# Kernel tuning notes

Hardware: AMD Instinct MI355X
Metric: run time of the kernel (lower is better)

The kernel has to match this reference:

```python
import jax, jax.numpy as jnp
import numpy as np

B, S, E, H = 2, 2048, 512, 8
MLP = 4 * E


def _ln(x, w, b, eps=1e-5):
    m = jnp.mean(x, -1, keepdims=True)
    v = jnp.var(x, -1, keepdims=True)
    return (x - m) / jnp.sqrt(v + eps) * w + b


def setup_inputs() -> dict:
    key = jax.random.key(0)
    ks = jax.random.split(key, 8)
    s = lambda k, shape: (jax.random.normal(k, shape, jnp.float32) * 0.02)
    return {
        "query": jax.random.normal(ks[0], (B, S, E), jnp.float32),
        "attn_gate": jax.random.uniform(ks[1], (B * H, S, S), jnp.float32),
        "in_proj_w": s(ks[2], (3 * E, E)),
        "in_proj_b": jnp.zeros((3 * E,), jnp.float32),
        "out_w": s(ks[3], (E, E)),
        "out_b": jnp.zeros((E,), jnp.float32),
        "ln1_w": jnp.ones((E,), jnp.float32),
        "ln1_b": jnp.zeros((E,), jnp.float32),
        "ln2_w": jnp.ones((E,), jnp.float32),
        "ln2_b": jnp.zeros((E,), jnp.float32),
        "w1": s(ks[4], (MLP, E)),
        "b1": jnp.zeros((MLP,), jnp.float32),
        "w2": s(ks[5], (E, MLP)),
        "b2": jnp.zeros((E,), jnp.float32),
    }


def reference(query, attn_gate, in_proj_w, in_proj_b, out_w, out_b,
              ln1_w, ln1_b, ln2_w, ln2_b, w1, b1, w2, b2):
    b, s, e = query.shape
    h = H
    dh = e // h
    nq = _ln(query, ln1_w, ln1_b)  # pre-LN; key=value=normed query (self-attn)
    Wq, Wk, Wv = jnp.split(in_proj_w, 3, axis=0)
    bq, bk, bv = jnp.split(in_proj_b, 3, axis=0)
    q = nq @ Wq.T + bq
    k = nq @ Wk.T + bk
    v = nq @ Wv.T + bv
    # faithful raw reshape (B,S,E)->(B*H,S,Dh), as in the torch .view
    q = q.reshape(b * h, s, dh)
    k = k.reshape(b * h, s, dh)
    v = v.reshape(b * h, s, dh)
    w = jnp.einsum("bqd,bkd->bqk", q, k)  # no 1/sqrt(d) scaling in source
    w = w * attn_gate
    w = w / (jnp.sum(w, -1, keepdims=True) + 1e-12)  # sum-renormalization
    w = jax.nn.softmax(w, axis=-1)
    o = jnp.einsum("bqk,bkd->bqd", w, v)  # (B*H, S, Dh)
    o = jnp.swapaxes(o, 0, 1).reshape(s, b, e)  # faithful transpose+view
    o = o @ out_w.T + out_b
    o = jnp.swapaxes(o, 0, 1)  # back to batch_first (B,S,E)
    x = query + o
    hmid = _ln(x, ln2_w, ln2_b)
    x = x + (jax.nn.gelu(hmid @ w1.T + b1, approximate=False) @ w2.T + b2)
    attn_weights = w.reshape(b, h, s, s).mean(axis=1)  # average_attn_weights=True
    return (x, attn_weights)
```

## Files before the change

kernel.cpp:

```cpp
#include <hip/hip_runtime.h>
#include <cstdint>
#include <cstddef>

typedef __bf16 bf16_t;
typedef __bf16 bf16x8 __attribute__((ext_vector_type(8)));
typedef float  f32x4  __attribute__((ext_vector_type(4)));

#define S_LEN   2048
#define E_DIM   512
#define H_NUM   8
#define DH      64
#define MLP_DIM 2048

static __device__ __forceinline__ unsigned short f2bfu(float f){
  bf16_t h = (bf16_t)f;
  return __builtin_bit_cast(unsigned short, h);
}

static __device__ __forceinline__ float gelu_f(float v){
  return 0.5f*v*(1.0f + erff(v*0.70710678118654752f));
}

__global__ __launch_bounds__(256) void cvt_kernel(const float* __restrict__ s,
                                                  bf16_t* __restrict__ d, int n){
  int i = (blockIdx.x*256 + threadIdx.x)*4;
  if (i < n){
    float4 v = *(const float4*)(s + i);
    ushort4 pk;
    pk.x = f2bfu(v.x); pk.y = f2bfu(v.y); pk.z = f2bfu(v.z); pk.w = f2bfu(v.w);
    *(ushort4*)((unsigned short*)d + i) = pk;
  }
}

__global__ __launch_bounds__(256) void cvt_split_kernel(const float* __restrict__ s,
                                                        bf16_t* __restrict__ dh,
                                                        bf16_t* __restrict__ dl, int n){
  int i = (blockIdx.x*256 + threadIdx.x)*4;
  if (i < n){
    float4 v = *(const float4*)(s + i);
    float xs[4] = {v.x, v.y, v.z, v.w};
    ushort4 ph, pl;
    unsigned short* hp = (unsigned short*)&ph;
    unsigned short* lp = (unsigned short*)&pl;
    #pragma unroll
    for (int j=0;j<4;j++){
      bf16_t hi = (bf16_t)xs[j];
      bf16_t lo = (bf16_t)(xs[j] - (float)hi);
      hp[j] = __builtin_bit_cast(unsigned short, hi);
      lp[j] = __builtin_bit_cast(unsigned short, lo);
    }
    *(ushort4*)((unsigned short*)dh + i) = ph;
    *(ushort4*)((unsigned short*)dl + i) = pl;
  }
}

__global__ __launch_bounds__(256) void ln_kernel(const float* __restrict__ x,
                                                 const float* __restrict__ w,
                                                 const float* __restrict__ bb,
                                                 bf16_t* __restrict__ out){
  const int row  = blockIdx.x*4 + (threadIdx.x>>6);
  const int lane = threadIdx.x & 63;
  const float* xr = x + (size_t)row*E_DIM + lane*8;
  float4 v0 = *(const float4*)xr;
  float4 v1 = *(const float4*)(xr + 4);
  float xs[8] = {v0.x, v0.y, v0.z, v0.w, v1.x, v1.y, v1.z, v1.w};
  float s = 0.f, s2 = 0.f;
  #pragma unroll
  for (int j=0;j<8;j++){ s += xs[j]; s2 += xs[j]*xs[j]; }
  #pragma unroll
  for (int off=1; off<64; off<<=1){
    s  += __shfl_xor(s,  off, 64);
    s2 += __shfl_xor(s2, off, 64);
  }
  float mean = s*(1.f/512.f);
  float var  = s2*(1.f/512.f) - mean*mean;
  float rstd = rsqrtf(fmaxf(var, 0.f) + 1e-5f);
  const float* wp = w  + lane*8;
  const float* bp = bb + lane*8;
  bf16x8 ov;
  #pragma unroll
  for (int j=0;j<8;j++)
    ov[j] = (bf16_t)((xs[j]-mean)*rstd*wp[j] + bp[j]);
  *(bf16x8*)(out + (size_t)row*E_DIM + lane*8) = ov;
}

__global__ __launch_bounds__(256) void ln_split_kernel(const float* __restrict__ x,
                                                       const float* __restrict__ w,
                                                       const float* __restrict__ bb,
                                                       bf16_t* __restrict__ oh,
                                                       bf16_t* __restrict__ ol){
  const int row  = blockIdx.x*4 + (threadIdx.x>>6);
  const int lane = threadIdx.x & 63;
  const float* xr = x + (size_t)row*E_DIM + lane*8;
  float4 v0 = *(const float4*)xr;
  float4 v1 = *(const float4*)(xr + 4);
  float xs[8] = {v0.x, v0.y, v0.z, v0.w, v1.x, v1.y, v1.z, v1.w};
  float s = 0.f, s2 = 0.f;
  #pragma unroll
  for (int j=0;j<8;j++){ s += xs[j]; s2 += xs[j]*xs[j]; }
  #pragma unroll
  for (int off=1; off<64; off<<=1){
    s  += __shfl_xor(s,  off, 64);
    s2 += __shfl_xor(s2, off, 64);
  }
  float mean = s*(1.f/512.f);
  float var  = s2*(1.f/512.f) - mean*mean;
  float rstd = rsqrtf(fmaxf(var, 0.f) + 1e-5f);
  const float* wp = w  + lane*8;
  const float* bp = bb + lane*8;
  bf16x8 vh, vl;
  #pragma unroll
  for (int j=0;j<8;j++){
    float v = (xs[j]-mean)*rstd*wp[j] + bp[j];
    bf16_t hi = (bf16_t)v;
    vh[j] = hi;
    vl[j] = (bf16_t)(v - (float)hi);
  }
  size_t o = (size_t)row*E_DIM + lane*8;
  *(bf16x8*)(oh + o) = vh;
  *(bf16x8*)(ol + o) = vl;
}

__global__ __launch_bounds__(256) void gemm_qkv_split(
    const bf16_t* __restrict__ Ah, const bf16_t* __restrict__ Al,
    const bf16_t* __restrict__ Bh, const bf16_t* __restrict__ Bl,
    const float* __restrict__ bias,
    bf16_t* __restrict__ qh, bf16_t* __restrict__ ql,
    bf16_t* __restrict__ kh, bf16_t* __restrict__ kl,
    bf16_t* __restrict__ vtmp)
{
  constexpr int TM = 128, TN = 64, BK = 64, MI = 4, NI = 2;
  const int K = 512;

  __shared__ bf16_t Ahs[TM*BK], Als[TM*BK];
  __shared__ bf16_t Bhs[TN*BK], Bls[TN*BK];

  const int tid  = threadIdx.x;
  const int wave = tid>>6, lane = tid&63, quad = lane>>4, l16 = lane&15;
  const int wm = wave>>1, wn = wave&1;

  const int nblk = 1536/TN;
  const int bm = blockIdx.x / nblk;
  const int bn = blockIdx.x % nblk;
  const int m0 = bm*TM, n0 = bn*TN;

  f32x4 acc[MI][NI];
  #pragma unroll
  for (int i=0;i<MI;i++)
    #pragma unroll
    for (int j=0;j<NI;j++)
      acc[i][j] = (f32x4){0.f,0.f,0.f,0.f};

  for (int k0 = 0; k0 < K; k0 += BK){
    bf16x8 avh[4], avl[4], bvh[2], bvl[2];
    #pragma unroll
    for (int i=0;i<4;i++){
      int ga = tid + i*256;
      int row = ga>>3, c8 = (ga&7) ^ (row&7);
      size_t off = (size_t)(m0+row)*K + k0 + c8*8;
      avh[i] = *(const bf16x8*)(Ah + off);
      avl[i] = *(const bf16x8*)(Al + off);
    }
    #pragma unroll
    for (int i=0;i<2;i++){
      int gb = tid + i*256;
      int row = gb>>3, c8 = (gb&7) ^ (row&7);
      size_t off = (size_t)(n0+row)*K + k0 + c8*8;
      bvh[i] = *(const bf16x8*)(Bh + off);
      bvl[i] = *(const bf16x8*)(Bl + off);
    }
    __syncthreads();
    #pragma unroll
    for (int i=0;i<4;i++){
      *(bf16x8*)(Ahs + (size_t)(tid + i*256)*8) = avh[i];
      *(bf16x8*)(Als + (size_t)(tid + i*256)*8) = avl[i];
    }
    #pragma unroll
    for (int i=0;i<2;i++){
      *(bf16x8*)(Bhs + (size_t)(tid + i*256)*8) = bvh[i];
      *(bf16x8*)(Bls + (size_t)(tid + i*256)*8) = bvl[i];
    }
    __syncthreads();
    #pragma unroll
    for (int ks=0;ks<2;ks++){
      bf16x8 afh[MI], afl[MI], bfh[NI], bfl[NI];
      #pragma unroll
      for (int mi=0;mi<MI;mi++){
        int rm = wm*64 + mi*16 + l16;
        size_t sl = (size_t)(rm*8 + ((ks*4+quad) ^ (rm&7)))*8;
        afh[mi] = *(const bf16x8*)(Ahs + sl);
        afl[mi] = *(const bf16x8*)(Als + sl);
      }
      #pragma unroll
      for (int ni=0;ni<NI;ni++){
        int rn = wn*32 + ni*16 + l16;
        size_t sl = (size_t)(rn*8 + ((ks*4+quad) ^ (rn&7)))*8;
        bfh[ni] = *(const bf16x8*)(Bhs + sl);
        bfl[ni] = *(const bf16x8*)(Bls + sl);
      }
      #pragma unroll
      for (int mi=0;mi<MI;mi++)
        #pragma unroll
        for (int ni=0;ni<NI;ni++){
          acc[mi][ni] = __builtin_amdgcn_mfma_f32_16x16x32_bf16(afh[mi], bfh[ni], acc[mi][ni], 0,0,0);
          acc[mi][ni] = __builtin_amdgcn_mfma_f32_16x16x32_bf16(afl[mi], bfh[ni], acc[mi][ni], 0,0,0);
          acc[mi][ni] = __builtin_amdgcn_mfma_f32_16x16x32_bf16(afh[mi], bfl[ni], acc[mi][ni], 0,0,0);
        }
    }
  }

  #pragma unroll
  for (int mi=0;mi<MI;mi++){
    const int grow0 = m0 + wm*64 + mi*16 + quad*4;
    #pragma unroll
    for (int ni=0;ni<NI;ni++){
      const int gcol = n0 + wn*32 + ni*16 + l16;
      const float bvx = bias[gcol];
      if (gcol < 512){
        #pragma unroll
        for (int r=0;r<4;r++){
          float v = acc[mi][ni][r] + bvx;
          size_t idx = (size_t)(grow0+r)*E_DIM + gcol;
          bf16_t hi = (bf16_t)v;
          qh[idx] = hi;
          ql[idx] = (bf16_t)(v - (float)hi);
        }
      } else if (gcol < 1024){
        const int cc = gcol - 512;
        #pragma unroll
        for (int r=0;r<4;r++){
          float v = acc[mi][ni][r] + bvx;
          size_t idx = (size_t)(grow0+r)*E_DIM + cc;
          bf16_t hi = (bf16_t)v;
          kh[idx] = hi;
          kl[idx] = (bf16_t)(v - (float)hi);
        }
      } else {
        const int cc = gcol - 1024;
        #pragma unroll
        for (int r=0;r<4;r++)
          vtmp[(size_t)(grow0+r)*E_DIM + cc] = (bf16_t)(acc[mi][ni][r] + bvx);
      }
    }
  }
}

__global__ __launch_bounds__(256) void vtrans_kernel(const bf16_t* __restrict__ v,
                                                     bf16_t* __restrict__ vt){
  __shared__ bf16_t tile[32*516];
  const int ic = blockIdx.x >> 3;
  const int rg = blockIdx.x & 7;
  const int tid = threadIdx.x;
  const size_t src = ((size_t)ic*256 + rg*32)*E_DIM;
  #pragma unroll
  for (int j=0;j<8;j++){
    int idx = j*2048 + tid*8;
    int row = idx >> 9, col = idx & 511;
    *(bf16x8*)(tile + row*516 + col) = *(const bf16x8*)(v + src + idx);
  }
  __syncthreads();
  #pragma unroll
  for (int j=0;j<8;j++){
    int idx = j*2048 + tid*8;
    int d = idx >> 8;
    int toff = idx & 255;
    int row = toff >> 3;
    bf16x8 o;
    #pragma unroll
    for (int jj=0;jj<8;jj++)
      o[jj] = tile[row*516 + jj*64 + d];
    *(bf16x8*)(vt + ((size_t)ic*64 + d)*S_LEN + rg*256 + toff) = o;
  }
}

template<int TN, int MODE>
__global__ __launch_bounds__(256) void gemm_kernel(
    const bf16_t* __restrict__ A, const bf16_t* __restrict__ Bw,
    const float* __restrict__ bias, int M, int N, int K,
    void* out0, const float* __restrict__ resid)
{
  constexpr int TM = 128;
  constexpr int BK = 64;
  constexpr int MI = 4;
  constexpr int NI = TN/32;
  constexpr int GB = TN/32;

  __shared__ bf16_t As[TM*BK];
  __shared__ bf16_t Bs[TN*BK];

  const int tid  = threadIdx.x;
  const int wave = tid>>6, lane = tid&63, quad = lane>>4, l16 = lane&15;
  const int wm = wave>>1, wn = wave&1;

  const int nblk = N / TN;
  const int bm = blockIdx.x / nblk;
  const int bn = blockIdx.x % nblk;
  const int m0 = bm*TM, n0 = bn*TN;

  f32x4 acc[MI][NI];
  #pragma unroll
  for (int i=0;i<MI;i++)
    #pragma unroll
    for (int j=0;j<NI;j++)
      acc[i][j] = (f32x4){0.f,0.f,0.f,0.f};

  for (int k0 = 0; k0 < K; k0 += BK){
    bf16x8 av[4];
    #pragma unroll
    for (int i=0;i<4;i++){
      int ga = tid + i*256;
      int row = ga>>3, c8 = (ga&7) ^ (row&7);
      av[i] = *(const bf16x8*)(A + (size_t)(m0+row)*K + k0 + c8*8);
    }
    bf16x8 bv[GB];
    #pragma unroll
    for (int i=0;i<GB;i++){
      int gb = tid + i*256;
      int row = gb>>3, c8 = (gb&7) ^ (row&7);
      bv[i] = *(const bf16x8*)(Bw + (size_t)(n0+row)*K + k0 + c8*8);
    }
    __syncthreads();
    #pragma unroll
    for (int i=0;i<4;i++)  *(bf16x8*)(As + (size_t)(tid + i*256)*8) = av[i];
    #pragma unroll
    for (int i=0;i<GB;i++) *(bf16x8*)(Bs + (size_t)(tid + i*256)*8) = bv[i];
    __syncthreads();
    #pragma unroll
    for (int ks=0;ks<2;ks++){
      bf16x8 af[MI], bfr[NI];
      #pragma unroll
      for (int mi=0;mi<MI;mi++){
        int rm = wm*64 + mi*16 + l16;
        af[mi] = *(const bf16x8*)(As + (size_t)(rm*8 + ((ks*4+quad) ^ (rm&7)))*8);
      }
      #pragma unroll
      for (int ni=0;ni<NI;ni++){
        int rn = wn*(TN/2) + ni*16 + l16;
        bfr[ni] = *(const bf16x8*)(Bs + (size_t)(rn*8 + ((ks*4+quad) ^ (rn&7)))*8);
      }
      #pragma unroll
      for (int mi=0;mi<MI;mi++)
        #pragma unroll
        for (int ni=0;ni<NI;ni++)
          acc[mi][ni] = __builtin_amdgcn_mfma_f32_16x16x32_bf16(af[mi], bfr[ni], acc[mi][ni], 0,0,0);
    }
  }

  #pragma unroll
  for (int mi=0;mi<MI;mi++){
    const int grow0 = m0 + wm*64 + mi*16 + quad*4;
    #pragma unroll
    for (int ni=0;ni<NI;ni++){
      const int gcol = n0 + wn*(TN/2) + ni*16 + l16;
      const float bvx = bias[gcol];
      if constexpr (MODE==1){
        float* xo = (float*)out0;
        #pragma unroll
        for (int r=0;r<4;r++){
          size_t idx = (size_t)(grow0+r)*E_DIM + gcol;
          xo[idx] = resid[idx] + acc[mi][ni][r] + bvx;
        }
      } else if constexpr (MODE==2){
        bf16_t* hp = (bf16_t*)out0;
        #pragma unroll
        for (int r=0;r<4;r++)
          hp[(size_t)(grow0+r)*MLP_DIM + gcol] = (bf16_t)gelu_f(acc[mi][ni][r] + bvx);
      } else {
        float* xo = (float*)out0;
        #pragma unroll
        for (int r=0;r<4;r++){
          size_t idx = (size_t)(grow0+r)*E_DIM + gcol;
          xo[idx] = xo[idx] + acc[mi][ni][r] + bvx;
        }
      }
    }
  }
}

__global__ __launch_bounds__(512) __attribute__((amdgpu_waves_per_eu(2, 2)))
void attn_kernel(
    const bf16_t* __restrict__ qhb, const bf16_t* __restrict__ qlb,
    const bf16_t* __restrict__ khb, const bf16_t* __restrict__ klb,
    const bf16_t* __restrict__ vt,  const float* __restrict__ gate,
    bf16_t* __restrict__ og, float* __restrict__ aw)
{
  __shared__ __align__(16) float u_s[16*2048];
  __shared__ float osh[16*64];
  __shared__ float zsh[16];

  const int b   = blockIdx.x >> 7;
  const int sqt = blockIdx.x & 127;
  const int sq0 = sqt*16;

  const int tid = threadIdx.x;
  const int wave = tid>>6, lane = tid&63, quad = lane>>4, l16 = lane&15;

  float awacc[64];
  #pragma unroll
  for (int j=0;j<64;j++) awacc[j] = 0.f;

  f32x4 gpre[2][8];
  #pragma unroll
  for (int rr=0;rr<2;rr++){
    const float* gp = gate + ((size_t)(b*H_NUM)*S_LEN + sq0 + wave*2 + rr)*S_LEN + (size_t)lane*4;
    #pragma unroll
    for (int it=0; it<8; it++)
      gpre[rr][it] = __builtin_nontemporal_load((const f32x4*)(gp + it*256));
  }

  for (int h = 0; h < H_NUM; h++){
    const int bh = b*H_NUM + h;

    osh[tid] = 0.f; osh[tid + 512] = 0.f;

    bf16x8 qah0, qah1, qal0, qal1;
    {
      const size_t qoff = ((size_t)bh*S_LEN + sq0 + l16)*DH + quad*8;
      qah0 = *(const bf16x8*)(qhb + qoff);
      qah1 = *(const bf16x8*)(qhb + qoff + 32);
      qal0 = *(const bf16x8*)(qlb + qoff);
      qal1 = *(const bf16x8*)(qlb + qoff + 32);
    }

    for (int cb = wave; cb < 32; cb += 8){
      #pragma unroll
      for (int nb=0; nb<4; nb++){
        const int col0 = cb*64 + nb*16;
        const size_t koff = ((size_t)bh*S_LEN + col0 + l16)*DH + quad*8;
        bf16x8 khf0 = *(const bf16x8*)(khb + koff);
        bf16x8 khf1 = *(const bf16x8*)(khb + koff + 32);
        bf16x8 klf0 = *(const bf16x8*)(klb + koff);
        bf16x8 klf1 = *(const bf16x8*)(klb + koff + 32);
        f32x4 acc = (f32x4){0.f,0.f,0.f,0.f};
        acc = __builtin_amdgcn_mfma_f32_16x16x32_bf16(qah0, khf0, acc, 0,0,0);
        acc = __builtin_amdgcn_mfma_f32_16x16x32_bf16(qah1, khf1, acc, 0,0,0);
        acc = __builtin_amdgcn_mfma_f32_16x16x32_bf16(qal0, khf0, acc, 0,0,0);
        acc = __builtin_amdgcn_mfma_f32_16x16x32_bf16(qal1, khf1, acc, 0,0,0);
        acc = __builtin_amdgcn_mfma_f32_16x16x32_bf16(qah0, klf0, acc, 0,0,0);
        acc = __builtin_amdgcn_mfma_f32_16x16x32_bf16(qah1, klf1, acc, 0,0,0);
        const int c = col0 + l16;
        #pragma unroll
        for (int r=0;r<4;r++){
          const int row = quad*4 + r;
          u_s[row*2048 + (c ^ ((row&7)<<2))] = acc[r];
        }
      }
    }
    __syncthreads();

    #pragma unroll
    for (int rr=0; rr<2; rr++){
      const int row = wave*2 + rr;
      f32x4* ub = (f32x4*)u_s + (size_t)row*512;
      const int sw = row & 7;
      f32x4 uv[8];
      double s = 0.0;
      float mx = -__builtin_inff(), mn = __builtin_inff();
      #pragma unroll
      for (int it=0; it<8; it++){
        uv[it] = ub[(it*64 + lane) ^ sw] * gpre[rr][it];
        s += ((double)uv[it][0] + (double)uv[it][1]) + ((double)uv[it][2] + (double)uv[it][3]);
        mx = fmaxf(mx, fmaxf(fmaxf(uv[it][0],uv[it][1]), fmaxf(uv[it][2],uv[it][3])));
        mn = fminf(mn, fminf(fminf(uv[it][0],uv[it][1]), fminf(uv[it][2],uv[it][3])));
      }
      #pragma unroll
      for (int off=1; off<64; off<<=1){
        s  += __shfl_xor(s, off, 64);
        mx = fmaxf(mx, __shfl_xor(mx, off, 64));
        mn = fminf(mn, __shfl_xor(mn, off, 64));
      }
      const double rsum = s + 1e-12;
      const float inv = (float)(1.0/rsum);
      const float m = (rsum > 0.0 ? mx : mn) * inv;
      float z = 0.f;
      #pragma unroll
      for (int it=0; it<8; it++){
        f32x4 e;
        e[0] = __expf(uv[it][0]*inv - m);
        e[1] = __expf(uv[it][1]*inv - m);
        e[2] = __expf(uv[it][2]*inv - m);
        e[3] = __expf(uv[it][3]*inv - m);
        ub[(it*64 + lane) ^ sw] = e;
        z += (e[0]+e[1]) + (e[2]+e[3]);
      }
      #pragma unroll
      for (int off=1; off<64; off<<=1) z += __shfl_xor(z, off, 64);
      if (lane == 0) zsh[row] = z;
    }
    __syncthreads();

    {
      const int nb2 = wave & 3, khh = wave >> 2;
      f32x4 oacc = (f32x4){0.f,0.f,0.f,0.f};
      const bf16_t* vbase = vt + ((size_t)bh*DH + nb2*16 + l16)*S_LEN;
      const f32x4* ur4 = (const f32x4*)u_s + (size_t)l16*512;
      const int swr = l16 & 7;
      #pragma unroll 4
      for (int kc = khh*32; kc < khh*32 + 32; kc++){
        const int c4a = kc*8 + quad*2;
        f32x4 e0 = ur4[c4a ^ swr];
        f32x4 e1 = ur4[(c4a+1) ^ swr];
        bf16x8 pa;
        pa[0]=(bf16_t)e0[0]; pa[1]=(bf16_t)e0[1]; pa[2]=(bf16_t)e0[2]; pa[3]=(bf16_t)e0[3];
        pa[4]=(bf16_t)e1[0]; pa[5]=(bf16_t)e1[1]; pa[6]=(bf16_t)e1[2]; pa[7]=(bf16_t)e1[3];
        bf16x8 vf = *(const bf16x8*)(vbase + kc*32 + quad*8);
        oacc = __builtin_amdgcn_mfma_f32_16x16x32_bf16(pa, vf, oacc, 0,0,0);
      }
      #pragma unroll
      for (int r=0;r<4;r++)
        atomicAdd(&osh[(quad*4+r)*64 + nb2*16 + l16], oacc[r]);
    }
    __syncthreads();

    #pragma unroll
    for (int t = tid; t < 1024; t += 512){
      int r = t >> 6, d = t & 63;
      float val = osh[t] / zsh[r];
      og[((size_t)(b*S_LEN + sq0 + r))*E_DIM + h*DH + d] = (bf16_t)val;
    }

    if (h + 1 < H_NUM){
      #pragma unroll
      for (int rr=0;rr<2;rr++){
        const float* gp = gate + ((size_t)(b*H_NUM + h + 1)*S_LEN + sq0 + wave*2 + rr)*S_LEN + (size_t)lane*4;
        #pragma unroll
        for (int it=0; it<8; it++)
          gpre[rr][it] = __builtin_nontemporal_load((const f32x4*)(gp + it*256));
      }
    }

    #pragma unroll
    for (int rr=0; rr<2; rr++){
      const int row = wave*2 + rr;
      const float sc = 0.125f / zsh[row];
      const f32x4* ur3 = (const f32x4*)u_s + (size_t)row*512;
      const int sw3 = row & 7;
      #pragma unroll
      for (int g=0; g<8; g++){
        f32x4 e = ur3[(g*64 + lane) ^ sw3];
        awacc[rr*32+g*4+0] = fmaf(e[0], sc, awacc[rr*32+g*4+0]);
        awacc[rr*32+g*4+1] = fmaf(e[1], sc, awacc[rr*32+g*4+1]);
        awacc[rr*32+g*4+2] = fmaf(e[2], sc, awacc[rr*32+g*4+2]);
        awacc[rr*32+g*4+3] = fmaf(e[3], sc, awacc[rr*32+g*4+3]);
      }
    }
    __syncthreads();
  }

  #pragma unroll
  for (int rr=0; rr<2; rr++){
    float* awrow = aw + ((size_t)(b*S_LEN) + sq0 + wave*2 + rr)*S_LEN + (size_t)lane*4;
    #pragma unroll
    for (int g=0; g<8; g++){
      f32x4 v = (f32x4){ awacc[rr*32+g*4+0], awacc[rr*32+g*4+1],
                         awacc[rr*32+g*4+2], awacc[rr*32+g*4+3] };
      __builtin_nontemporal_store(v, (f32x4*)(awrow + g*256));
    }
  }
}

extern "C" void kernel_launch(void* const* d_in, const int* in_sizes, int n_in,
                              void* d_out, int out_size, void* d_ws, size_t ws_size,
                              hipStream_t stream)
{
  const float* query     = (const float*)d_in[0];
  const float* gate      = (const float*)d_in[1];
  const float* in_proj_w = (const float*)d_in[2];
  const float* in_proj_b = (const float*)d_in[3];
  const float* out_w     = (const float*)d_in[4];
  const float* out_b     = (const float*)d_in[5];
  const float* ln1_w     = (const float*)d_in[6];
  const float* ln1_b     = (const float*)d_in[7];
  const float* ln2_w     = (const float*)d_in[8];
  const float* ln2_b     = (const float*)d_in[9];
  const float* w1        = (const float*)d_in[10];
  const float* b1        = (const float*)d_in[11];
  const float* w2        = (const float*)d_in[12];
  const float* b2        = (const float*)d_in[13];

  char* ws = (char*)d_ws;
  bf16_t* nqh   = (bf16_t*)(ws);
  bf16_t* nql   = (bf16_t*)(ws + ((size_t)4<<20));
  bf16_t* qh    = (bf16_t*)(ws + ((size_t)8<<20));
  bf16_t* ql    = (bf16_t*)(ws + ((size_t)12<<20));
  bf16_t* kh    = (bf16_t*)(ws + ((size_t)16<<20));
  bf16_t* kl    = (bf16_t*)(ws + ((size_t)20<<20));
  bf16_t* vtmp  = (bf16_t*)(ws + ((size_t)24<<20));
  bf16_t* vt    = (bf16_t*)(ws + ((size_t)28<<20));
  bf16_t* og    = (bf16_t*)(ws + ((size_t)32<<20));
  bf16_t* hmid  = (bf16_t*)(ws + ((size_t)36<<20));
  bf16_t* h1    = (bf16_t*)(ws + ((size_t)40<<20));
  bf16_t* wqh   = (bf16_t*)(ws + ((size_t)56<<20));
  bf16_t* wql   = (bf16_t*)(ws + ((size_t)58<<20));
  bf16_t* woutb = (bf16_t*)(ws + ((size_t)60<<20));
  bf16_t* w1b   = (bf16_t*)(ws + ((size_t)61<<20));
  bf16_t* w2b   = (bf16_t*)(ws + ((size_t)63<<20));

  float* xout = (float*)d_out;
  float* aw   = xout + (size_t)2*S_LEN*E_DIM;

  cvt_split_kernel<<<768, 256, 0, stream>>>(in_proj_w, wqh, wql, 786432);
  cvt_kernel<<<256, 256, 0, stream>>>(out_w, woutb, 262144);
  cvt_kernel<<<1024,256, 0, stream>>>(w1,    w1b,   1048576);
  cvt_kernel<<<1024,256, 0, stream>>>(w2,    w2b,   1048576);

  ln_split_kernel<<<1024, 256, 0, stream>>>(query, ln1_w, ln1_b, nqh, nql);

  gemm_qkv_split<<<768, 256, 0, stream>>>(nqh, nql, wqh, wql, in_proj_b,
                                          qh, ql, kh, kl, vtmp);

  vtrans_kernel<<<128, 256, 0, stream>>>(vtmp, vt);

  attn_kernel<<<256, 512, 0, stream>>>(qh, ql, kh, kl, vt, gate, og, aw);

  gemm_kernel<64,1><<<256, 256, 0, stream>>>(og, woutb, out_b,
      4096, 512, 512, (void*)xout, query);

  ln_kernel<<<1024, 256, 0, stream>>>(xout, ln2_w, ln2_b, hmid);

  gemm_kernel<128,2><<<512, 256, 0, stream>>>(hmid, w1b, b1,
      4096, 2048, 512, (void*)h1, nullptr);

  gemm_kernel<64,3><<<256, 256, 0, stream>>>(h1, w2b, b2,
      4096, 512, 2048, (void*)xout, nullptr);
}
```

Baseline: 705.8 us.

## Halve attention query tile to 8 rows to double blocks and occupancy

The attention kernel now handles 8 query rows per block instead of 16 and launches 512 blocks. That halves LDS use (64KB instead of 128KB), the awacc registers and the gate prefetch registers, and the waves-per-EU hint goes from 2 to 4. The MFMA tiles stay 16 wide, so half of each QK and PV tile is wasted work on duplicated rows. The next head's gate prefetch moves earlier into the softmax pass, and the gated scores are written back to LDS instead of being held in registers.

```diff
diff --git a/kernel.cpp b/kernel.cpp
--- a/kernel.cpp
+++ b/kernel.cpp
@@ -377,45 +377,44 @@
   }
 }
 
-__global__ __launch_bounds__(512) __attribute__((amdgpu_waves_per_eu(2, 2)))
+__global__ __launch_bounds__(512) __attribute__((amdgpu_waves_per_eu(4, 4)))
 void attn_kernel(
     const bf16_t* __restrict__ qhb, const bf16_t* __restrict__ qlb,
     const bf16_t* __restrict__ khb, const bf16_t* __restrict__ klb,
     const bf16_t* __restrict__ vt,  const float* __restrict__ gate,
     bf16_t* __restrict__ og, float* __restrict__ aw)
 {
-  __shared__ __align__(16) float u_s[16*2048];
-  __shared__ float osh[16*64];
-  __shared__ float zsh[16];
-
-  const int b   = blockIdx.x >> 7;
-  const int sqt = blockIdx.x & 127;
-  const int sq0 = sqt*16;
+  __shared__ __align__(16) float u_s[8*2048];
+  __shared__ float osh[8*64];
+  __shared__ float zsh[8];
+
+  const int b   = blockIdx.x >> 8;
+  const int sqt = blockIdx.x & 255;
+  const int sq0 = sqt*8;
 
   const int tid = threadIdx.x;
   const int wave = tid>>6, lane = tid&63, quad = lane>>4, l16 = lane&15;
 
-  float awacc[64];
-  #pragma unroll
-  for (int j=0;j<64;j++) awacc[j] = 0.f;
-
-  f32x4 gpre[2][8];
-  #pragma unroll
-  for (int rr=0;rr<2;rr++){
-    const float* gp = gate + ((size_t)(b*H_NUM)*S_LEN + sq0 + wave*2 + rr)*S_LEN + (size_t)lane*4;
+  float awacc[32];
+  #pragma unroll
+  for (int j=0;j<32;j++) awacc[j] = 0.f;
+
+  f32x4 gpre[8];
+  {
+    const float* gp = gate + ((size_t)(b*H_NUM)*S_LEN + sq0 + wave)*S_LEN + (size_t)lane*4;
     #pragma unroll
     for (int it=0; it<8; it++)
-      gpre[rr][it] = __builtin_nontemporal_load((const f32x4*)(gp + it*256));
+      gpre[it] = *(const f32x4*)(gp + it*256);
   }
 
   for (int h = 0; h < H_NUM; h++){
     const int bh = b*H_NUM + h;
 
-    osh[tid] = 0.f; osh[tid + 512] = 0.f;
+    osh[tid] = 0.f;
 
     bf16x8 qah0, qah1, qal0, qal1;
     {
-      const size_t qoff = ((size_t)bh*S_LEN + sq0 + l16)*DH + quad*8;
+      const size_t qoff = ((size_t)bh*S_LEN + sq0 + (l16&7))*DH + quad*8;
       qah0 = *(const bf16x8*)(qhb + qoff);
       qah1 = *(const bf16x8*)(qhb + qoff + 32);
       qal0 = *(const bf16x8*)(qlb + qoff);
@@ -439,29 +438,37 @@
         acc = __builtin_amdgcn_mfma_f32_16x16x32_bf16(qah0, klf0, acc, 0,0,0);
         acc = __builtin_amdgcn_mfma_f32_16x16x32_bf16(qah1, klf1, acc, 0,0,0);
         const int c = col0 + l16;
-        #pragma unroll
-        for (int r=0;r<4;r++){
-          const int row = quad*4 + r;
-          u_s[row*2048 + (c ^ ((row&7)<<2))] = acc[r];
+        if (quad < 2){
+          #pragma unroll
+          for (int r=0;r<4;r++){
+            const int row = quad*4 + r;
+            u_s[row*2048 + (c ^ (row<<2))] = acc[r];
+          }
         }
       }
     }
     __syncthreads();
 
-    #pragma unroll
-    for (int rr=0; rr<2; rr++){
-      const int row = wave*2 + rr;
+    {
+      const int row = wave;
       f32x4* ub = (f32x4*)u_s + (size_t)row*512;
-      const int sw = row & 7;
-      f32x4 uv[8];
+      const int sw = row;
       double s = 0.0;
       float mx = -__builtin_inff(), mn = __builtin_inff();
       #pragma unroll
       for (int it=0; it<8; it++){
-        uv[it] = ub[(it*64 + lane) ^ sw] * gpre[rr][it];
-        s += ((double)uv[it][0] + (double)uv[it][1]) + ((double)uv[it][2] + (double)uv[it][3]);
-        mx = fmaxf(mx, fmaxf(fmaxf(uv[it][0],uv[it][1]), fmaxf(uv[it][2],uv[it][3])));
-        mn = fminf(mn, fminf(fminf(uv[it][0],uv[it][1]), fminf(uv[it][2],uv[it][3])));
+        const int c4 = (it*64 + lane) ^ sw;
+        f32x4 u = ub[c4] * gpre[it];
+        ub[c4] = u;
+        s += ((double)u[0] + (double)u[1]) + ((double)u[2] + (double)u[3]);
+        mx = fmaxf(mx, fmaxf(fmaxf(u[0],u[1]), fmaxf(u[2],u[3])));
+        mn = fminf(mn, fminf(fminf(u[0],u[1]), fminf(u[2],u[3])));
+      }
+      if (h + 1 < H_NUM){
+        const float* gp = gate + ((size_t)(b*H_NUM + h + 1)*S_LEN + sq0 + wave)*S_LEN + (size_t)lane*4;
+        #pragma unroll
+        for (int it=0; it<8; it++)
+          gpre[it] = *(const f32x4*)(gp + it*256);
       }
       #pragma unroll
       for (int off=1; off<64; off<<=1){
@@ -475,12 +482,14 @@
       float z = 0.f;
       #pragma unroll
       for (int it=0; it<8; it++){
+        const int c4 = (it*64 + lane) ^ sw;
+        f32x4 u = ub[c4];
         f32x4 e;
-        e[0] = __expf(uv[it][0]*inv - m);
-        e[1] = __expf(uv[it][1]*inv - m);
-        e[2] = __expf(uv[it][2]*inv - m);
-        e[3] = __expf(uv[it][3]*inv - m);
-        ub[(it*64 + lane) ^ sw] = e;
+        e[0] = __expf(u[0]*inv - m);
+        e[1] = __expf(u[1]*inv - m);
+        e[2] = __expf(u[2]*inv - m);
+        e[3] = __expf(u[3]*inv - m);
+        ub[c4] = e;
         z += (e[0]+e[1]) + (e[2]+e[3]);
       }
       #pragma unroll
@@ -493,7 +502,7 @@
       const int nb2 = wave & 3, khh = wave >> 2;
       f32x4 oacc = (f32x4){0.f,0.f,0.f,0.f};
       const bf16_t* vbase = vt + ((size_t)bh*DH + nb2*16 + l16)*S_LEN;
-      const f32x4* ur4 = (const f32x4*)u_s + (size_t)l16*512;
+      const f32x4* ur4 = (const f32x4*)u_s + (size_t)(l16&7)*512;
       const int swr = l16 & 7;
       #pragma unroll 4
       for (int kc = khh*32; kc < khh*32 + 32; kc++){
@@ -506,54 +515,42 @@
         bf16x8 vf = *(const bf16x8*)(vbase + kc*32 + quad*8);
         oacc = __builtin_amdgcn_mfma_f32_16x16x32_bf16(pa, vf, oacc, 0,0,0);
       }
-      #pragma unroll
-      for (int r=0;r<4;r++)
-        atomicAdd(&osh[(quad*4+r)*64 + nb2*16 + l16], oacc[r]);
-    }
-    __syncthreads();
-
-    #pragma unroll
-    for (int t = tid; t < 1024; t += 512){
-      int r = t >> 6, d = t & 63;
-      float val = osh[t] / zsh[r];
+      if (quad < 2){
+        #pragma unroll
+        for (int r=0;r<4;r++)
+          atomicAdd(&osh[(quad*4+r)*64 + nb2*16 + l16], oacc[r]);
+      }
+    }
+    __syncthreads();
+
+    {
+      int r = tid >> 6, d = tid & 63;
+      float val = osh[tid] / zsh[r];
       og[((size_t)(b*S_LEN + sq0 + r))*E_DIM + h*DH + d] = (bf16_t)val;
     }
 
-    if (h + 1 < H_NUM){
-      #pragma unroll
-      for (int rr=0;rr<2;rr++){
-        const float* gp = gate + ((size_t)(b*H_NUM + h + 1)*S_LEN + sq0 + wave*2 + rr)*S_LEN + (size_t)lane*4;
-        #pragma unroll
-        for (int it=0; it<8; it++)
-          gpre[rr][it] = __builtin_nontemporal_load((const f32x4*)(gp + it*256));
-      }
-    }
-
-    #pragma unroll
-    for (int rr=0; rr<2; rr++){
-      const int row = wave*2 + rr;
+    {
+      const int row = wave;
       const float sc = 0.125f / zsh[row];
       const f32x4* ur3 = (const f32x4*)u_s + (size_t)row*512;
-      const int sw3 = row & 7;
+      const int sw3 = row;
       #pragma unroll
       for (int g=0; g<8; g++){
         f32x4 e = ur3[(g*64 + lane) ^ sw3];
-        awacc[rr*32+g*4+0] = fmaf(e[0], sc, awacc[rr*32+g*4+0]);
-        awacc[rr*32+g*4+1] = fmaf(e[1], sc, awacc[rr*32+g*4+1]);
-        awacc[rr*32+g*4+2] = fmaf(e[2], sc, awacc[rr*32+g*4+2]);
-        awacc[rr*32+g*4+3] = fmaf(e[3], sc, awacc[rr*32+g*4+3]);
-      }
-    }
-    __syncthreads();
-  }
-
-  #pragma unroll
-  for (int rr=0; rr<2; rr++){
-    float* awrow = aw + ((size_t)(b*S_LEN) + sq0 + wave*2 + rr)*S_LEN + (size_t)lane*4;
+        awacc[g*4+0] = fmaf(e[0], sc, awacc[g*4+0]);
+        awacc[g*4+1] = fmaf(e[1], sc, awacc[g*4+1]);
+        awacc[g*4+2] = fmaf(e[2], sc, awacc[g*4+2]);
+        awacc[g*4+3] = fmaf(e[3], sc, awacc[g*4+3]);
+      }
+    }
+    __syncthreads();
+  }
+
+  {
+    float* awrow = aw + ((size_t)(b*S_LEN) + sq0 + wave)*S_LEN + (size_t)lane*4;
     #pragma unroll
     for (int g=0; g<8; g++){
-      f32x4 v = (f32x4){ awacc[rr*32+g*4+0], awacc[rr*32+g*4+1],
-                         awacc[rr*32+g*4+2], awacc[rr*32+g*4+3] };
+      f32x4 v = (f32x4){ awacc[g*4+0], awacc[g*4+1], awacc[g*4+2], awacc[g*4+3] };
       __builtin_nontemporal_store(v, (f32x4*)(awrow + g*256));
     }
   }
@@ -611,7 +608,7 @@
 
   vtrans_kernel<<<128, 256, 0, stream>>>(vtmp, vt);
 
-  attn_kernel<<<256, 512, 0, stream>>>(qh, ql, kh, kl, vt, gate, og, aw);
+  attn_kernel<<<512, 512, 0, stream>>>(qh, ql, kh, kl, vt, gate, og, aw);
 
   gemm_kernel<64,1><<<256, 256, 0, stream>>>(og, woutb, out_b,
       4096, 512, 512, (void*)xout, query);
```

New measurement: 899.8 us. 27.5% more time.
